# Kernel optimization log

Hardware: AMD Instinct MI355X
Metric: run time of the kernel (lower is better)

Reference implementation:

```python
import jax, jax.numpy as jnp
import numpy as np


def setup_inputs() -> dict:
    key = jax.random.key(0)
    k1, k2 = jax.random.split(key)
    B, N, M, D = 1, 4096, 4096, 32
    i1 = jax.random.normal(k1, (B, N, D), dtype=jnp.float32)
    i2 = jax.random.normal(k2, (B, M, D), dtype=jnp.float32)
    return {"i1": i1, "i2": i2}


def reference(i1, i2):
    # Faithful to tf: exp(-sum((i1[..., :, None, :] - i2[..., None, :, :])**2, -1) / 2)
    d = i1[..., :, None, :] - i2[..., None, :, :]   # [B, N, M, D]
    sq = jnp.sum(d * d, axis=-1)                    # [B, N, M]
    return jnp.exp(-sq / 2.0)
```

## Files before the change

### kernel.cpp

```cpp
#include <hip/hip_runtime.h>


#define D 32
#define BT 128
#define LDT 132

__global__ __launch_bounds__(256, 4) void rbf_tile_kernel(
    const float* __restrict__ A,
    const float* __restrict__ B,
    float* __restrict__ out,
    int M)
{
    __shared__ float sA[D][LDT];
    __shared__ float sB[D][LDT];
    __shared__ float hnA[BT];
    __shared__ float hnB[BT];

    const int tid  = threadIdx.x;
    const int brow = blockIdx.y * BT;
    const int bcol = blockIdx.x * BT;

    const float4* gA = reinterpret_cast<const float4*>(A + brow * D);
    const float4* gB = reinterpret_cast<const float4*>(B + bcol * D);
    #pragma unroll
    for (int k = 0; k < 4; ++k) {
        const int i   = tid + k * 256;
        const int row = i >> 3;
        const int d0  = (i & 7) << 2;
        float4 va = gA[i];
        float4 vb = gB[i];
        sA[d0 + 0][row] = va.x; sA[d0 + 1][row] = va.y;
        sA[d0 + 2][row] = va.z; sA[d0 + 3][row] = va.w;
        sB[d0 + 0][row] = vb.x; sB[d0 + 1][row] = vb.y;
        sB[d0 + 2][row] = vb.z; sB[d0 + 3][row] = vb.w;
    }
    __syncthreads();

    if (tid < BT) {
        float s = 0.f;
        #pragma unroll
        for (int d = 0; d < D; ++d) { float v = sA[d][tid]; s += v * v; }
        hnA[tid] = 0.5f * s;
    } else {
        const int r = tid - BT;
        float s = 0.f;
        #pragma unroll
        for (int d = 0; d < D; ++d) { float v = sB[d][r]; s += v * v; }
        hnB[r] = 0.5f * s;
    }
    __syncthreads();

    const int g   = tid >> 4;
    const int c   = tid & 15;
    const int tr  = g * 8;
    const int tc0 = c * 4;
    const int tc1 = c * 4 + 64;

    float acc[8][8];
    #pragma unroll
    for (int i = 0; i < 8; ++i)
        #pragma unroll
        for (int j = 0; j < 8; ++j) acc[i][j] = 0.f;

    #pragma unroll
    for (int d = 0; d < D; ++d) {
        const float4 a0 = *reinterpret_cast<const float4*>(&sA[d][tr]);
        const float4 a1 = *reinterpret_cast<const float4*>(&sA[d][tr + 4]);
        const float4 b0 = *reinterpret_cast<const float4*>(&sB[d][tc0]);
        const float4 b1 = *reinterpret_cast<const float4*>(&sB[d][tc1]);
        const float av[8] = {a0.x, a0.y, a0.z, a0.w, a1.x, a1.y, a1.z, a1.w};
        const float bv[8] = {b0.x, b0.y, b0.z, b0.w, b1.x, b1.y, b1.z, b1.w};
        #pragma unroll
        for (int i = 0; i < 8; ++i)
            #pragma unroll
            for (int j = 0; j < 8; ++j)
                acc[i][j] += av[i] * bv[j];
    }

    float hna[8], hnb[8];
    #pragma unroll
    for (int i = 0; i < 8; ++i) hna[i] = hnA[tr + i];
    #pragma unroll
    for (int j = 0; j < 4; ++j) { hnb[j] = hnB[tc0 + j]; hnb[j + 4] = hnB[tc1 + j]; }

    #pragma unroll
    for (int i = 0; i < 8; ++i) {
        const float h = hna[i];
        float4 o0, o1;
        o0.x = __expf(acc[i][0] - h - hnb[0]);
        o0.y = __expf(acc[i][1] - h - hnb[1]);
        o0.z = __expf(acc[i][2] - h - hnb[2]);
        o0.w = __expf(acc[i][3] - h - hnb[3]);
        o1.x = __expf(acc[i][4] - h - hnb[4]);
        o1.y = __expf(acc[i][5] - h - hnb[5]);
        o1.z = __expf(acc[i][6] - h - hnb[6]);
        o1.w = __expf(acc[i][7] - h - hnb[7]);
        float* r = out + (size_t)(brow + tr + i) * M + bcol;
        *reinterpret_cast<float4*>(r + tc0) = o0;
        *reinterpret_cast<float4*>(r + tc1) = o1;
    }
}

extern "C" void kernel_launch(void* const* d_in, const int* in_sizes, int n_in,
                              void* d_out, int out_size, void* d_ws, size_t ws_size,
                              hipStream_t stream) {
    const float* A = (const float*)d_in[0];
    const float* B = (const float*)d_in[1];
    float* out     = (float*)d_out;
    const int N = in_sizes[0] / D;
    const int M = in_sizes[1] / D;
    dim3 grid(M / BT, N / BT);
    rbf_tile_kernel<<<grid, 256, 0, stream>>>(A, B, out, M);
}
```

Measured before the change: 86.76 us.

## Process two column tiles per block, prefetching the second B tile during compute

Each block now handles a 128x256 output region as two sequential 128x128 tiles. The A tile and its norms are reused across both tiles. The second B tile is loaded into registers before the first tile's compute and written to a second shared buffer afterwards, so global load latency overlaps with FMA and exp work. This halves the block count and drops the occupancy hint of 4 from launch_bounds. Shared memory use goes up, which may lower occupancy or hurt scheduling on a kernel that is largely bound by output writes.

```diff
diff --git a/kernel.cpp b/kernel.cpp
--- a/kernel.cpp
+++ b/kernel.cpp
@@ -5,34 +5,40 @@
 #define BT 128
 #define LDT 132
 
-__global__ __launch_bounds__(256, 4) void rbf_tile_kernel(
+__global__ __launch_bounds__(256) void rbf_pipe_kernel(
     const float* __restrict__ A,
     const float* __restrict__ B,
     float* __restrict__ out,
-    int M)
+    int M, int colpairs)
 {
     __shared__ float sA[D][LDT];
-    __shared__ float sB[D][LDT];
+    __shared__ float sB[2][D][LDT];
     __shared__ float hnA[BT];
-    __shared__ float hnB[BT];
+    __shared__ float hnB[2][BT];
 
-    const int tid  = threadIdx.x;
-    const int brow = blockIdx.y * BT;
-    const int bcol = blockIdx.x * BT;
+    const int tid = threadIdx.x;
+    const int b   = blockIdx.x;
+    const int rr_ = b / colpairs;
+    const int cp  = b % colpairs;
+    const int brow  = rr_ * BT;
+    const int bcol0 = cp * (2 * BT);
+    const int bcol1 = bcol0 + BT;
 
-    const float4* gA = reinterpret_cast<const float4*>(A + brow * D);
-    const float4* gB = reinterpret_cast<const float4*>(B + bcol * D);
+    const float4* gA  = reinterpret_cast<const float4*>(A + (size_t)brow  * D);
+    const float4* gB0 = reinterpret_cast<const float4*>(B + (size_t)bcol0 * D);
+    const float4* gB1 = reinterpret_cast<const float4*>(B + (size_t)bcol1 * D);
+
     #pragma unroll
     for (int k = 0; k < 4; ++k) {
         const int i   = tid + k * 256;
         const int row = i >> 3;
         const int d0  = (i & 7) << 2;
         float4 va = gA[i];
-        float4 vb = gB[i];
-        sA[d0 + 0][row] = va.x; sA[d0 + 1][row] = va.y;
-        sA[d0 + 2][row] = va.z; sA[d0 + 3][row] = va.w;
-        sB[d0 + 0][row] = vb.x; sB[d0 + 1][row] = vb.y;
-        sB[d0 + 2][row] = vb.z; sB[d0 + 3][row] = vb.w;
+        float4 vb = gB0[i];
+        sA[d0+0][row] = va.x; sA[d0+1][row] = va.y;
+        sA[d0+2][row] = va.z; sA[d0+3][row] = va.w;
+        sB[0][d0+0][row] = vb.x; sB[0][d0+1][row] = vb.y;
+        sB[0][d0+2][row] = vb.z; sB[0][d0+3][row] = vb.w;
     }
     __syncthreads();
 
@@ -42,11 +48,11 @@
         for (int d = 0; d < D; ++d) { float v = sA[d][tid]; s += v * v; }
         hnA[tid] = 0.5f * s;
     } else {
-        const int r = tid - BT;
+        const int rw = tid - BT;
         float s = 0.f;
         #pragma unroll
-        for (int d = 0; d < D; ++d) { float v = sB[d][r]; s += v * v; }
-        hnB[r] = 0.5f * s;
+        for (int d = 0; d < D; ++d) { float v = sB[0][d][rw]; s += v * v; }
+        hnB[0][rw] = 0.5f * s;
     }
     __syncthreads();
 
@@ -56,49 +62,80 @@
     const int tc0 = c * 4;
     const int tc1 = c * 4 + 64;
 
-    float acc[8][8];
+    float4 pb[4];
     #pragma unroll
-    for (int i = 0; i < 8; ++i)
-        #pragma unroll
-        for (int j = 0; j < 8; ++j) acc[i][j] = 0.f;
+    for (int k = 0; k < 4; ++k) pb[k] = gB1[tid + k * 256];
 
-    #pragma unroll
-    for (int d = 0; d < D; ++d) {
-        const float4 a0 = *reinterpret_cast<const float4*>(&sA[d][tr]);
-        const float4 a1 = *reinterpret_cast<const float4*>(&sA[d][tr + 4]);
-        const float4 b0 = *reinterpret_cast<const float4*>(&sB[d][tc0]);
-        const float4 b1 = *reinterpret_cast<const float4*>(&sB[d][tc1]);
-        const float av[8] = {a0.x, a0.y, a0.z, a0.w, a1.x, a1.y, a1.z, a1.w};
-        const float bv[8] = {b0.x, b0.y, b0.z, b0.w, b1.x, b1.y, b1.z, b1.w};
+    auto do_tile = [&](const float (*sBt)[LDT], const float* hnBt, int bcolt) {
+        float acc[8][8];
         #pragma unroll
         for (int i = 0; i < 8; ++i)
             #pragma unroll
-            for (int j = 0; j < 8; ++j)
-                acc[i][j] += av[i] * bv[j];
-    }
+            for (int j = 0; j < 8; ++j) acc[i][j] = 0.f;
 
-    float hna[8], hnb[8];
-    #pragma unroll
-    for (int i = 0; i < 8; ++i) hna[i] = hnA[tr + i];
-    #pragma unroll
-    for (int j = 0; j < 4; ++j) { hnb[j] = hnB[tc0 + j]; hnb[j + 4] = hnB[tc1 + j]; }
+        #pragma unroll 4
+        for (int d = 0; d < D; ++d) {
+            const float4 a0 = *reinterpret_cast<const float4*>(&sA[d][tr]);
+            const float4 a1 = *reinterpret_cast<const float4*>(&sA[d][tr + 4]);
+            const float4 b0 = *reinterpret_cast<const float4*>(&sBt[d][tc0]);
+            const float4 b1 = *reinterpret_cast<const float4*>(&sBt[d][tc1]);
+            const float av[8] = {a0.x, a0.y, a0.z, a0.w, a1.x, a1.y, a1.z, a1.w};
+            const float bv[8] = {b0.x, b0.y, b0.z, b0.w, b1.x, b1.y, b1.z, b1.w};
+            #pragma unroll
+            for (int i = 0; i < 8; ++i)
+                #pragma unroll
+                for (int j = 0; j < 8; ++j)
+                    acc[i][j] += av[i] * bv[j];
+        }
+
+        float hnb[8];
+        #pragma unroll
+        for (int j = 0; j < 4; ++j) { hnb[j] = hnBt[tc0 + j]; hnb[j + 4] = hnBt[tc1 + j]; }
+
+        #pragma unroll
+        for (int i = 0; i < 8; ++i) {
+            const float h = hnA[tr + i];
+            float4 o0, o1;
+            o0.x = __expf(acc[i][0] - h - hnb[0]);
+            o0.y = __expf(acc[i][1] - h - hnb[1]);
+            o0.z = __expf(acc[i][2] - h - hnb[2]);
+            o0.w = __expf(acc[i][3] - h - hnb[3]);
+            o1.x = __expf(acc[i][4] - h - hnb[4]);
+            o1.y = __expf(acc[i][5] - h - hnb[5]);
+            o1.z = __expf(acc[i][6] - h - hnb[6]);
+            o1.w = __expf(acc[i][7] - h - hnb[7]);
+            float* rp = out + (size_t)(brow + tr + i) * M + bcolt;
+            *reinterpret_cast<float4*>(rp + tc0) = o0;
+            *reinterpret_cast<float4*>(rp + tc1) = o1;
+        }
+    };
+
+    do_tile(sB[0], hnB[0], bcol0);
 
     #pragma unroll
-    for (int i = 0; i < 8; ++i) {
-        const float h = hna[i];
-        float4 o0, o1;
-        o0.x = __expf(acc[i][0] - h - hnb[0]);
-        o0.y = __expf(acc[i][1] - h - hnb[1]);
-        o0.z = __expf(acc[i][2] - h - hnb[2]);
-        o0.w = __expf(acc[i][3] - h - hnb[3]);
-        o1.x = __expf(acc[i][4] - h - hnb[4]);
-        o1.y = __expf(acc[i][5] - h - hnb[5]);
-        o1.z = __expf(acc[i][6] - h - hnb[6]);
-        o1.w = __expf(acc[i][7] - h - hnb[7]);
-        float* r = out + (size_t)(brow + tr + i) * M + bcol;
-        *reinterpret_cast<float4*>(r + tc0) = o0;
-        *reinterpret_cast<float4*>(r + tc1) = o1;
+    for (int k = 0; k < 4; ++k) {
+        const int i   = tid + k * 256;
+        const int row = i >> 3;
+        const int d0  = (i & 7) << 2;
+        sB[1][d0+0][row] = pb[k].x; sB[1][d0+1][row] = pb[k].y;
+        sB[1][d0+2][row] = pb[k].z; sB[1][d0+3][row] = pb[k].w;
     }
+    asm volatile("s_waitcnt lgkmcnt(0)" ::: "memory");
+    __builtin_amdgcn_s_barrier();
+    asm volatile("" ::: "memory");
+
+    if (tid >= BT) {
+        const int rw = tid - BT;
+        float s = 0.f;
+        #pragma unroll
+        for (int d = 0; d < D; ++d) { float v = sB[1][d][rw]; s += v * v; }
+        hnB[1][rw] = 0.5f * s;
+    }
+    asm volatile("s_waitcnt lgkmcnt(0)" ::: "memory");
+    __builtin_amdgcn_s_barrier();
+    asm volatile("" ::: "memory");
+
+    do_tile(sB[1], hnB[1], bcol1);
 }
 
 extern "C" void kernel_launch(void* const* d_in, const int* in_sizes, int n_in,
@@ -109,6 +146,7 @@
     float* out     = (float*)d_out;
     const int N = in_sizes[0] / D;
     const int M = in_sizes[1] / D;
-    dim3 grid(M / BT, N / BT);
-    rbf_tile_kernel<<<grid, 256, 0, stream>>>(A, B, out, M);
+    const int colpairs = M / (2 * BT);
+    const int nblocks  = (N / BT) * colpairs;
+    rbf_pipe_kernel<<<nblocks, 256, 0, stream>>>(A, B, out, M, colpairs);
 }
```

New measurement: 88.38 us. Within noise of the previous version (+1.9%).

## Compute RBF dot products with split-bf16 MFMA instead of FP32 FMA

Applied to the files above, without the earlier changes.

Replaces the FP32 register-tiled outer-product loop with MFMA 16x16x32 bf16 instructions. Each input is split into high and low bf16 parts, and three MFMAs per tile recover near-FP32 accuracy. Row norms are now computed straight from global memory and packed into spare LDS padding columns. The aim is to move the compute onto the matrix cores. In exchange, the output stores become scalar, strided by row in the MFMA layout rather than float4, and some precision is lost from dropping the low*low term.

```diff
diff --git a/kernel.cpp b/kernel.cpp
--- a/kernel.cpp
+++ b/kernel.cpp
@@ -1,103 +1,119 @@
 #include <hip/hip_runtime.h>
 
 
-#define D 32
+#define DD 32
 #define BT 128
-#define LDT 132
+#define KP 40
 
-__global__ __launch_bounds__(256, 4) void rbf_tile_kernel(
+typedef __attribute__((ext_vector_type(8))) short bfrag8;
+typedef __attribute__((ext_vector_type(4))) float f32x4;
+
+__device__ __forceinline__ unsigned short f2bf_rn(float f) {
+    unsigned u = __builtin_bit_cast(unsigned, f);
+    u += 0x7FFFu + ((u >> 16) & 1u);
+    return (unsigned short)(u >> 16);
+}
+__device__ __forceinline__ float bf2f(unsigned short h) {
+    unsigned u = ((unsigned)h) << 16;
+    return __builtin_bit_cast(float, u);
+}
+
+__global__ __launch_bounds__(256) void rbf_mfma_kernel(
     const float* __restrict__ A,
     const float* __restrict__ B,
     float* __restrict__ out,
     int M)
 {
-    __shared__ float sA[D][LDT];
-    __shared__ float sB[D][LDT];
-    __shared__ float hnA[BT];
-    __shared__ float hnB[BT];
+    __shared__ unsigned short sAh[BT][KP];
+    __shared__ unsigned short sAl[BT][KP];
+    __shared__ unsigned short sBh[BT][KP];
+    __shared__ unsigned short sBl[BT][KP];
 
     const int tid  = threadIdx.x;
     const int brow = blockIdx.y * BT;
     const int bcol = blockIdx.x * BT;
 
-    const float4* gA = reinterpret_cast<const float4*>(A + brow * D);
-    const float4* gB = reinterpret_cast<const float4*>(B + bcol * D);
+    const float4* gA = reinterpret_cast<const float4*>(A + (size_t)brow * DD);
+    const float4* gB = reinterpret_cast<const float4*>(B + (size_t)bcol * DD);
+
     #pragma unroll
     for (int k = 0; k < 4; ++k) {
         const int i   = tid + k * 256;
         const int row = i >> 3;
         const int d0  = (i & 7) << 2;
-        float4 va = gA[i];
-        float4 vb = gB[i];
-        sA[d0 + 0][row] = va.x; sA[d0 + 1][row] = va.y;
-        sA[d0 + 2][row] = va.z; sA[d0 + 3][row] = va.w;
-        sB[d0 + 0][row] = vb.x; sB[d0 + 1][row] = vb.y;
-        sB[d0 + 2][row] = vb.z; sB[d0 + 3][row] = vb.w;
+        float4 va = gA[i], vb = gB[i];
+        ushort4 ha, la, hb, lb;
+        ha.x = f2bf_rn(va.x); la.x = f2bf_rn(va.x - bf2f(ha.x));
+        ha.y = f2bf_rn(va.y); la.y = f2bf_rn(va.y - bf2f(ha.y));
+        ha.z = f2bf_rn(va.z); la.z = f2bf_rn(va.z - bf2f(ha.z));
+        ha.w = f2bf_rn(va.w); la.w = f2bf_rn(va.w - bf2f(ha.w));
+        hb.x = f2bf_rn(vb.x); lb.x = f2bf_rn(vb.x - bf2f(hb.x));
+        hb.y = f2bf_rn(vb.y); lb.y = f2bf_rn(vb.y - bf2f(hb.y));
+        hb.z = f2bf_rn(vb.z); lb.z = f2bf_rn(vb.z - bf2f(hb.z));
+        hb.w = f2bf_rn(vb.w); lb.w = f2bf_rn(vb.w - bf2f(hb.w));
+        *reinterpret_cast<ushort4*>(&sAh[row][d0]) = ha;
+        *reinterpret_cast<ushort4*>(&sAl[row][d0]) = la;
+        *reinterpret_cast<ushort4*>(&sBh[row][d0]) = hb;
+        *reinterpret_cast<ushort4*>(&sBl[row][d0]) = lb;
+    }
+
+    {
+        const int r = tid & 127;
+        const float4* src = (tid < 128)
+            ? reinterpret_cast<const float4*>(A + (size_t)(brow + r) * DD)
+            : reinterpret_cast<const float4*>(B + (size_t)(bcol + r) * DD);
+        float s = 0.f;
+        #pragma unroll
+        for (int q = 0; q < 8; ++q) {
+            float4 v = src[q];
+            s += v.x * v.x + v.y * v.y + v.z * v.z + v.w * v.w;
+        }
+        unsigned short* dst = (tid < 128) ? &sAh[r][32] : &sBh[r][32];
+        *reinterpret_cast<float*>(dst) = 0.5f * s;
     }
     __syncthreads();
 
-    if (tid < BT) {
-        float s = 0.f;
-        #pragma unroll
-        for (int d = 0; d < D; ++d) { float v = sA[d][tid]; s += v * v; }
-        hnA[tid] = 0.5f * s;
-    } else {
-        const int r = tid - BT;
-        float s = 0.f;
-        #pragma unroll
-        for (int d = 0; d < D; ++d) { float v = sB[d][r]; s += v * v; }
-        hnB[r] = 0.5f * s;
+    const int lane = tid & 63, wid = tid >> 6;
+    const int r0 = wid * 32;
+    const int lr = lane & 15;
+    const int lg = lane >> 4;
+    const int k0 = lg * 8;
+
+    const bfrag8 ah0 = *reinterpret_cast<const bfrag8*>(&sAh[r0 + lr][k0]);
+    const bfrag8 al0 = *reinterpret_cast<const bfrag8*>(&sAl[r0 + lr][k0]);
+    const bfrag8 ah1 = *reinterpret_cast<const bfrag8*>(&sAh[r0 + 16 + lr][k0]);
+    const bfrag8 al1 = *reinterpret_cast<const bfrag8*>(&sAl[r0 + 16 + lr][k0]);
+
+    float hna0[4], hna1[4];
+    #pragma unroll
+    for (int q = 0; q < 4; ++q) {
+        hna0[q] = *reinterpret_cast<const float*>(&sAh[r0 + lg * 4 + q][32]);
+        hna1[q] = *reinterpret_cast<const float*>(&sAh[r0 + 16 + lg * 4 + q][32]);
     }
-    __syncthreads();
 
-    const int g   = tid >> 4;
-    const int c   = tid & 15;
-    const int tr  = g * 8;
-    const int tc0 = c * 4;
-    const int tc1 = c * 4 + 64;
-
-    float acc[8][8];
-    #pragma unroll
-    for (int i = 0; i < 8; ++i)
-        #pragma unroll
-        for (int j = 0; j < 8; ++j) acc[i][j] = 0.f;
+    const size_t orow0 = (size_t)(brow + r0 + lg * 4) * M + bcol;
 
     #pragma unroll
-    for (int d = 0; d < D; ++d) {
-        const float4 a0 = *reinterpret_cast<const float4*>(&sA[d][tr]);
-        const float4 a1 = *reinterpret_cast<const float4*>(&sA[d][tr + 4]);
-        const float4 b0 = *reinterpret_cast<const float4*>(&sB[d][tc0]);
-        const float4 b1 = *reinterpret_cast<const float4*>(&sB[d][tc1]);
-        const float av[8] = {a0.x, a0.y, a0.z, a0.w, a1.x, a1.y, a1.z, a1.w};
-        const float bv[8] = {b0.x, b0.y, b0.z, b0.w, b1.x, b1.y, b1.z, b1.w};
+    for (int c = 0; c < 8; ++c) {
+        const int c0 = c * 16;
+        const bfrag8 bh = *reinterpret_cast<const bfrag8*>(&sBh[c0 + lr][k0]);
+        const bfrag8 bl = *reinterpret_cast<const bfrag8*>(&sBl[c0 + lr][k0]);
+        const float hnb = *reinterpret_cast<const float*>(&sBh[c0 + lr][32]);
+
+        f32x4 acc0 = {0.f, 0.f, 0.f, 0.f}, acc1 = {0.f, 0.f, 0.f, 0.f};
+        acc0 = __builtin_amdgcn_mfma_f32_16x16x32_bf16(al0, bh, acc0, 0, 0, 0);
+        acc1 = __builtin_amdgcn_mfma_f32_16x16x32_bf16(al1, bh, acc1, 0, 0, 0);
+        acc0 = __builtin_amdgcn_mfma_f32_16x16x32_bf16(ah0, bl, acc0, 0, 0, 0);
+        acc1 = __builtin_amdgcn_mfma_f32_16x16x32_bf16(ah1, bl, acc1, 0, 0, 0);
+        acc0 = __builtin_amdgcn_mfma_f32_16x16x32_bf16(ah0, bh, acc0, 0, 0, 0);
+        acc1 = __builtin_amdgcn_mfma_f32_16x16x32_bf16(ah1, bh, acc1, 0, 0, 0);
+
+        float* p0 = out + orow0 + c0 + lr;
         #pragma unroll
-        for (int i = 0; i < 8; ++i)
-            #pragma unroll
-            for (int j = 0; j < 8; ++j)
-                acc[i][j] += av[i] * bv[j];
-    }
-
-    float hna[8], hnb[8];
-    #pragma unroll
-    for (int i = 0; i < 8; ++i) hna[i] = hnA[tr + i];
-    #pragma unroll
-    for (int j = 0; j < 4; ++j) { hnb[j] = hnB[tc0 + j]; hnb[j + 4] = hnB[tc1 + j]; }
-
-    #pragma unroll
-    for (int i = 0; i < 8; ++i) {
-        const float h = hna[i];
-        float4 o0, o1;
-        o0.x = __expf(acc[i][0] - h - hnb[0]);
-        o0.y = __expf(acc[i][1] - h - hnb[1]);
-        o0.z = __expf(acc[i][2] - h - hnb[2]);
-        o0.w = __expf(acc[i][3] - h - hnb[3]);
-        o1.x = __expf(acc[i][4] - h - hnb[4]);
-        o1.y = __expf(acc[i][5] - h - hnb[5]);
-        o1.z = __expf(acc[i][6] - h - hnb[6]);
-        o1.w = __expf(acc[i][7] - h - hnb[7]);
-        float* r = out + (size_t)(brow + tr + i) * M + bcol;
-        *reinterpret_cast<float4*>(r + tc0) = o0;
-        *reinterpret_cast<float4*>(r + tc1) = o1;
+        for (int q = 0; q < 4; ++q) {
+            p0[(size_t)q * M]        = __expf(acc0[q] - hna0[q] - hnb);
+            p0[(size_t)(q + 16) * M] = __expf(acc1[q] - hna1[q] - hnb);
+        }
     }
 }
 
@@ -107,8 +123,8 @@
     const float* A = (const float*)d_in[0];
     const float* B = (const float*)d_in[1];
     float* out     = (float*)d_out;
-    const int N = in_sizes[0] / D;
-    const int M = in_sizes[1] / D;
+    const int N = in_sizes[0] / DD;
+    const int M = in_sizes[1] / DD;
     dim3 grid(M / BT, N / BT);
-    rbf_tile_kernel<<<grid, 256, 0, stream>>>(A, B, out, M);
+    rbf_mfma_kernel<<<grid, 256, 0, stream>>>(A, B, out, M);
 }
```

Result: faster. 81.84 us (median of 2 runs) (-5.7%).
